# Performance work log

Hardware: AMD Instinct MI355X
Metric: run time of the kernel (lower is better)

Reference implementation:

```python
import jax, jax.numpy as jnp
import numpy as np

C_STD = 64                 # len(standard_1020)
CH_NUMS = (1, 4, 16, 64)   # multi-scale channel counts (ms_ch_lst / ch_nums)
BETA = 0.25
DECAY = 0.99
RESI = 0.5                 # abs(quant_resi) for shared Phi


def l2norm(t, eps=1e-12):
    return t / jnp.maximum(jnp.linalg.norm(t, axis=-1, keepdims=True), eps)


def phi_apply(h_LND, w, b):
    # Phi: y = (1-r)*h + r*Conv1d(h), conv over the channel-position axis, feature dim D
    x = jnp.swapaxes(h_LND, 1, 2)                      # (L, D, Nch)
    y = jax.lax.conv_general_dilated(x, w, (1,), 'SAME',
                                     dimension_numbers=('NCH', 'OIH', 'NCH'))
    y = y + b[None, :, None]
    y = jnp.swapaxes(y, 1, 2)                          # (L, Nch, D)
    return h_LND * (1.0 - RESI) + y * RESI


def setup_inputs() -> dict:
    key = jax.random.key(0)
    ks = jax.random.split(key, 5)
    B, T, D, V = 64, 16, 256, 8192
    N = T * C_STD
    z = jax.random.normal(ks[0], (B, N, D), jnp.float32)
    # per-sample permutation of the 64 standard channel ids in the first C_STD slots
    perm = jnp.argsort(jax.random.uniform(ks[1], (B, C_STD)), axis=1).astype(jnp.int32)
    input_chans = jnp.concatenate([perm, jnp.zeros((B, N - C_STD), jnp.int32)], axis=1)
    # tokens ordered time-major: token j has time index j // C_STD
    input_time = jnp.broadcast_to((jnp.arange(N) // C_STD)[None, :], (B, N)).astype(jnp.int32)
    embedding = jax.random.normal(ks[2], (V, D), jnp.float32) * (D ** -0.5 / 36.0)
    phi_w = jax.random.normal(ks[3], (D, D, 3), jnp.float32) * (1.0 / np.sqrt(3.0 * D))
    phi_b = jnp.zeros((D,), jnp.float32)
    cluster_size = jnp.zeros((V,), jnp.float32)
    return {"z": z, "input_chans": input_chans, "input_time": input_time,
            "embedding": embedding, "phi_w": phi_w, "phi_b": phi_b,
            "cluster_size": cluster_size}


def reference(z, input_chans, input_time, embedding, phi_w, phi_b, cluster_size):
    B, N, D = z.shape
    T = N // C_STD
    V = embedding.shape[0]
    z = l2norm(z)
    chans = input_chans[:, :C_STD]                     # (B, 64) channel ids
    # ch_trans: scatter tokens into standard channel layout -> (L, C_STD, D), L = B*T
    z_btcd = z.reshape(B, T, C_STD, D)
    z_LND = jax.vmap(lambda zb, cb: jnp.zeros((T, C_STD, D), z.dtype).at[:, cb].set(zb))(z_btcd, chans)
    z_LND = z_LND.reshape(B * T, C_STD, D)
    L = B * T

    f_no_grad = jax.lax.stop_gradient(z_LND)
    f_rest = f_no_grad
    f_hat = jnp.zeros_like(f_rest)
    e_n = l2norm(embedding)                            # normalized codebook (V, D)

    SN = len(CH_NUMS)
    loss = jnp.zeros((), z.dtype)
    counts = jnp.zeros((V,), z.dtype)
    idx_list = []
    for g in CH_NUMS:                                  # multi-scale residual VQ over channels
        rest_g = f_rest.reshape(L, g, C_STD // g, D).mean(axis=2)   # group_chans_by_mean
        q = l2norm(rest_g)
        logits = jnp.einsum('lgd,vd->lgv', q, e_n)     # cosine sim == -0.5*l2 dist + const
        idx = jnp.argmax(logits, axis=-1)              # (L, g)
        idx_list.append(idx)
        h_g = e_n[idx]                                 # codebook lookup (L, g, D)
        h = jnp.repeat(h_g, C_STD // g, axis=1)        # expand_chans_by_copy -> (L, 64, D)
        h = phi_apply(h, phi_w, phi_b)                 # shared Phi residual conv
        f_hat = f_hat + h
        f_rest = f_rest - h
        loss = loss + BETA * jnp.mean((jax.lax.stop_gradient(f_hat) - z_LND) ** 2) \
                    + jnp.mean((f_hat - f_no_grad) ** 2)
        counts = counts.at[idx.reshape(-1)].add(1.0)   # EMA cluster-size scatter
    loss = loss / SN

    # straight-through: value = f_hat, gradient flows to z
    f_hat_st = jax.lax.stop_gradient(f_hat) + (z_LND - f_no_grad)
    # ch_intrans: gather back to original per-sample channel ordering
    zq_btcd = jax.vmap(lambda fb, cb: fb[:, cb])(f_hat_st.reshape(B, T, C_STD, D), chans)
    z_q = zq_btcd.reshape(B, N, D)

    cluster_size_new = DECAY * cluster_size + (1.0 - DECAY) * counts
    idx_all = jnp.concatenate(idx_list, axis=1)        # (L, sum(CH_NUMS))
    return z_q, loss, idx_all, cluster_size_new
```

## Files before the change

kernel.cpp:

```cpp
#include <hip/hip_runtime.h>

#define D_DIM 256
#define V_DIM 8192
#define L_DIM 1024
#define NROW 65536
#define NELEM 16777216

#define OUT_LOSS 16777216
#define OUT_IDX  16777217
#define OUT_CS   16864257

#define EN_OFF    ((size_t)0)
#define ENH_OFF   ((size_t)2097152)
#define ESUM_OFF  ((size_t)3145728)
#define E0_OFF    ((size_t)5242880)
#define E2_OFF    ((size_t)7340032)
#define WSUM_OFF  ((size_t)9437184)
#define W0_OFF    ((size_t)9502720)
#define W2_OFF    ((size_t)9568256)
#define FREST_OFF ((size_t)9633792)
#define QF_OFF    ((size_t)26411008)
#define QH_OFF    ((size_t)43188224)
#define PTOP_OFF  ((size_t)51576832)
#define IDXI_OFF  ((size_t)52625408)
#define CNT_OFF   ((size_t)52712448)
#define LOSSP_OFF ((size_t)52720640)
#define RNORM_OFF ((size_t)52722688)
#define INV_OFF   ((size_t)52788224)

typedef __attribute__((ext_vector_type(8))) short bf16x8;
typedef __attribute__((ext_vector_type(4))) float f32x4;

__device__ __forceinline__ unsigned int umaxu(unsigned int a, unsigned int b) { return a > b ? a : b; }
__device__ __forceinline__ unsigned int uminu(unsigned int a, unsigned int b) { return a < b ? a : b; }

__device__ __forceinline__ unsigned short f2b(float x) {
    unsigned int u = __float_as_uint(x);
    unsigned int r = (u + 0x7FFFu + ((u >> 16) & 1u)) >> 16;
    return (unsigned short)r;
}

__device__ __forceinline__ void gl_lds16(const void* g, void* l) {
    __builtin_amdgcn_global_load_lds(
        (const __attribute__((address_space(1))) unsigned int*)g,
        (__attribute__((address_space(3))) unsigned int*)l, 16, 0, 0);
}

__device__ __forceinline__ float blk_reduce_sum(float v, float* sb) {
#pragma unroll
    for (int off = 32; off; off >>= 1) v += __shfl_down(v, off, 64);
    const int w = threadIdx.x >> 6;
    if ((threadIdx.x & 63) == 0) sb[w] = v;
    __syncthreads();
    return sb[0] + sb[1] + sb[2] + sb[3];
}

__global__ void k_norm_embed(const float* __restrict__ emb, float* __restrict__ en,
                             unsigned short* __restrict__ enh) {
    __shared__ float sb[4];
    const int v = blockIdx.x, o = threadIdx.x;
    const float x = emb[(size_t)v * 256 + o];
    const float ss = blk_reduce_sum(x * x, sb);
    const float sc = 1.0f / fmaxf(sqrtf(ss), 1e-12f);
    const float y = x * sc;
    en[(size_t)v * 256 + o] = y;
    enh[(size_t)v * 256 + o] = f2b(y);
}

__global__ void k_prep_w(const float* __restrict__ pw, float* __restrict__ wsum,
                         float* __restrict__ w0, float* __restrict__ w2) {
    const int i = blockIdx.x * 256 + threadIdx.x;
    const float a = pw[(size_t)i * 3 + 0];
    const float b = pw[(size_t)i * 3 + 1];
    const float c = pw[(size_t)i * 3 + 2];
    wsum[i] = a + b + c; w0[i] = a; w2[i] = c;
}

__global__ __launch_bounds__(256) void k_phi_gemm(
    const float* __restrict__ en, const float* __restrict__ wsum,
    const float* __restrict__ w0, const float* __restrict__ w2,
    float* __restrict__ esum, float* __restrict__ e0, float* __restrict__ e2) {
    __shared__ __align__(16) float smem[4096];
    float (*As)[128] = (float (*)[128])smem;
    float (*Bs)[128] = (float (*)[128])(smem + 2048);
    const float* Bm; float* Cm;
    if (blockIdx.z == 0)      { Bm = wsum; Cm = esum; }
    else if (blockIdx.z == 1) { Bm = w0;   Cm = e0;   }
    else                      { Bm = w2;   Cm = e2;   }
    const int tid = threadIdx.x, tx = tid & 15, ty = tid >> 4;
    const int rowbase = blockIdx.x * 128, colbase = blockIdx.y * 128;
    float acc[8][8];
#pragma unroll
    for (int r = 0; r < 8; r++)
#pragma unroll
        for (int c = 0; c < 8; c++) acc[r][c] = 0.f;
    for (int kb = 0; kb < 256; kb += 16) {
        __syncthreads();
        {
            const int lr = tid >> 1, k0 = (tid & 1) << 3;
            const float4* ap = (const float4*)(en + ((size_t)(rowbase + lr)) * 256 + kb + k0);
            const float4 a0 = ap[0], a1 = ap[1];
            const float4* bp = (const float4*)(Bm + ((size_t)(colbase + lr)) * 256 + kb + k0);
            const float4 b0 = bp[0], b1 = bp[1];
            As[k0+0][lr]=a0.x; As[k0+1][lr]=a0.y; As[k0+2][lr]=a0.z; As[k0+3][lr]=a0.w;
            As[k0+4][lr]=a1.x; As[k0+5][lr]=a1.y; As[k0+6][lr]=a1.z; As[k0+7][lr]=a1.w;
            Bs[k0+0][lr]=b0.x; Bs[k0+1][lr]=b0.y; Bs[k0+2][lr]=b0.z; Bs[k0+3][lr]=b0.w;
            Bs[k0+4][lr]=b1.x; Bs[k0+5][lr]=b1.y; Bs[k0+6][lr]=b1.z; Bs[k0+7][lr]=b1.w;
        }
        __syncthreads();
#pragma unroll
        for (int k = 0; k < 16; k++) {
            const float4 av0 = *(const float4*)&As[k][ty << 3];
            const float4 av1 = *(const float4*)&As[k][(ty << 3) + 4];
            const float4 bv0 = *(const float4*)&Bs[k][tx << 3];
            const float4 bv1 = *(const float4*)&Bs[k][(tx << 3) + 4];
            const float a[8] = {av0.x, av0.y, av0.z, av0.w, av1.x, av1.y, av1.z, av1.w};
            const float b[8] = {bv0.x, bv0.y, bv0.z, bv0.w, bv1.x, bv1.y, bv1.z, bv1.w};
#pragma unroll
            for (int r = 0; r < 8; r++)
#pragma unroll
                for (int c = 0; c < 8; c++) acc[r][c] = fmaf(a[r], b[c], acc[r][c]);
        }
    }
#pragma unroll
    for (int r = 0; r < 8; r++) {
        float4 o0 = {acc[r][0], acc[r][1], acc[r][2], acc[r][3]};
        float4 o1 = {acc[r][4], acc[r][5], acc[r][6], acc[r][7]};
        float* cp = Cm + ((size_t)(rowbase + (ty << 3) + r)) * 256 + colbase + (tx << 3);
        *(float4*)cp = o0; *(float4*)(cp + 4) = o1;
    }
}

__global__ void k_invperm(const int* __restrict__ ichans, int* __restrict__ inv) {
    const int b = blockIdx.x, c = threadIdx.x;
    inv[(b << 6) + ichans[(b << 10) + c]] = c;
}

__global__ void k_scatter(const float* __restrict__ z, const int* __restrict__ ichans,
                          float* __restrict__ frest, float* __restrict__ rnorm) {
    __shared__ float sb[4];
    const int zrow = blockIdx.x;
    const int b = zrow >> 10, n = zrow & 1023;
    const int t = n >> 6, c = n & 63;
    const int o = threadIdx.x;
    const float x = z[(size_t)zrow * 256 + o];
    const float ss = blk_reduce_sum(x * x, sb);
    const float sc = 1.0f / fmaxf(sqrtf(ss), 1e-12f);
    const int ch = ichans[(b << 10) + c];
    frest[((size_t)(((b << 4) + t) * 64 + ch)) * 256 + o] = x * sc;
    if (o == 0) rnorm[zrow] = sc;
}

__global__ void k_groupq(const float* __restrict__ frest, float* __restrict__ qf,
                         unsigned short* __restrict__ qh, int g, int s) {
    __shared__ float sb[4];
    const int r = blockIdx.x;
    const int l = r / g, j = r - l * g;
    const int o = threadIdx.x;
    const float* base = frest + ((size_t)l * 64 + (size_t)j * s) * 256 + o;
    float acc = 0.f;
    for (int cc = 0; cc < s; cc++) acc += base[(size_t)cc * 256];
    acc *= (1.0f / (float)s);
    const float ss = blk_reduce_sum(acc * acc, sb);
    const float sc = 1.0f / fmaxf(sqrtf(ss), 1e-12f);
    const float qv = acc * sc;
    qf[(size_t)r * 256 + o] = qv;
    qh[(size_t)r * 256 + o] = f2b(qv);
}

__global__ __launch_bounds__(256, 3) void k_amax1(
    const unsigned short* __restrict__ qh, const unsigned short* __restrict__ enh,
    uint2* __restrict__ ptop, int NC, int colsPerChunk) {
    __shared__ unsigned short As[2][4096];
    __shared__ unsigned short Bs[2][4096];
    const int tid = threadIdx.x;
    const int lane = tid & 63;
    const int m = lane & 15, q4 = lane >> 4;
    const int w = tid >> 6;
    const int wr = w >> 1, wc = w & 1;
    const int rowbase = blockIdx.x * 128;
    const int chunk = blockIdx.y;
    const int colbase0 = chunk * colsPerChunk;
    const int srow = tid >> 2, sgr = tid & 3;

    const unsigned short* qa0 = qh + (size_t)(rowbase + srow) * 256 + sgr * 8;
    const unsigned short* qa1 = qa0 + 64 * 256;
    const unsigned short* eb0 = enh + (size_t)srow * 256 + sgr * 8;
    const unsigned short* eb1 = eb0 + 64 * 256;
    const int loff = tid * 8;

    unsigned int t1[4][4], t2[4][4];
    f32x4 acc[4][4];
#pragma unroll
    for (int i = 0; i < 4; i++)
#pragma unroll
        for (int r = 0; r < 4; r++) {
            t1[i][r] = 0u; t2[i][r] = 0u;
            acc[i][r] = (f32x4){1.25f, 1.25f, 1.25f, 1.25f};
        }

    const int nsteps = (colsPerChunk >> 7) * 8;
    {
        gl_lds16(qa0, &As[0][loff]);
        gl_lds16(qa1, &As[0][2048 + loff]);
        const size_t bgo = (size_t)colbase0 * 256;
        gl_lds16(eb0 + bgo, &Bs[0][loff]);
        gl_lds16(eb1 + bgo, &Bs[0][2048 + loff]);
    }
    for (int step = 0; step < nsteps; step++) {
        const int buf = step & 1;
        __syncthreads();
        if (step + 1 < nsteps) {
            const int kb1 = (step + 1) & 7;
            const int tile1 = (step + 1) >> 3;
            gl_lds16(qa0 + kb1 * 32, &As[buf ^ 1][loff]);
            gl_lds16(qa1 + kb1 * 32, &As[buf ^ 1][2048 + loff]);
            const size_t bgo = (size_t)(colbase0 + tile1 * 128) * 256 + kb1 * 32;
            gl_lds16(eb0 + bgo, &Bs[buf ^ 1][loff]);
            gl_lds16(eb1 + bgo, &Bs[buf ^ 1][2048 + loff]);
        }
        bf16x8 af[4], bfr[4];
#pragma unroll
        for (int i = 0; i < 4; i++)
            af[i] = *(const bf16x8*)&As[buf][(wr * 64 + i * 16 + m) * 32 + q4 * 8];
#pragma unroll
        for (int j = 0; j < 4; j++)
            bfr[j] = *(const bf16x8*)&Bs[buf][(wc * 64 + j * 16 + m) * 32 + q4 * 8];
#pragma unroll
        for (int i = 0; i < 4; i++)
#pragma unroll
            for (int j = 0; j < 4; j++)
                acc[i][j] = __builtin_amdgcn_mfma_f32_16x16x32_bf16(af[i], bfr[j], acc[i][j], 0, 0, 0);
        if ((step & 7) == 7) {
            const int colchunk = colbase0 + (step >> 3) * 128;
#pragma unroll
            for (int j = 0; j < 4; j++) {
                const unsigned int ct = 8191u - (unsigned int)(colchunk + wc * 64 + j * 16 + m);
#pragma unroll
                for (int i = 0; i < 4; i++)
#pragma unroll
                    for (int r = 0; r < 4; r++) {
                        const unsigned int cand =
                            (__float_as_uint(acc[i][j][r]) & 0xFFFFE000u) | (ct & 0x1FFFu);
                        const unsigned int nb1 = umaxu(t1[i][r], cand);
                        t2[i][r] = umaxu(t2[i][r], uminu(t1[i][r], cand));
                        t1[i][r] = nb1;
                        acc[i][j][r] = 1.25f;
                    }
            }
        }
    }
    unsigned int mb1[4][4], mb2[4][4];
#pragma unroll
    for (int i = 0; i < 4; i++)
#pragma unroll
        for (int r = 0; r < 4; r++) {
            unsigned int b1 = t1[i][r], b2 = t2[i][r];
#pragma unroll
            for (int d = 1; d < 16; d <<= 1) {
                const unsigned int o1 = (unsigned int)__shfl_xor((int)b1, d, 64);
                const unsigned int o2 = (unsigned int)__shfl_xor((int)b2, d, 64);
                const unsigned int mn = uminu(b1, o1);
                b1 = umaxu(b1, o1);
                b2 = umaxu(mn, umaxu(b2, o2));
            }
            mb1[i][r] = b1; mb2[i][r] = b2;
        }
    __syncthreads();
    uint2* msh = (uint2*)&As[0][0];
    if (wc == 1 && m == 0) {
#pragma unroll
        for (int i = 0; i < 4; i++)
#pragma unroll
            for (int r = 0; r < 4; r++)
                msh[wr * 64 + i * 16 + q4 * 4 + r] = make_uint2(mb1[i][r], mb2[i][r]);
    }
    __syncthreads();
    if (wc == 0 && m == 0) {
#pragma unroll
        for (int i = 0; i < 4; i++)
#pragma unroll
            for (int r = 0; r < 4; r++) {
                const int rl = wr * 64 + i * 16 + q4 * 4 + r;
                const uint2 o = msh[rl];
                unsigned int b1 = mb1[i][r], b2 = mb2[i][r];
                const unsigned int mn = uminu(b1, o.x);
                b1 = umaxu(b1, o.x);
                b2 = umaxu(mn, umaxu(b2, o.y));
                ptop[(size_t)(rowbase + rl) * NC + chunk] = make_uint2(b1, b2);
            }
    }
}

__global__ __launch_bounds__(256) void k_amax2(
    const uint2* __restrict__ ptop, const float* __restrict__ qf,
    const float* __restrict__ en, int* __restrict__ idxout,
    float* __restrict__ counts, int R, int NC) {
    __shared__ uint2 stop;
    __shared__ double swv[4];
    __shared__ int swi[4];
    const int r = blockIdx.x;
    const int tid = threadIdx.x, lane = tid & 63, w = tid >> 6;
    const uint2* pp = ptop + (size_t)r * NC;
    if (w == 0) {
        const uint2 p = (lane < NC) ? pp[lane] : make_uint2(0u, 0u);
        unsigned int b1 = p.x, b2 = p.y;
#pragma unroll
        for (int d = 1; d < 64; d <<= 1) {
            const unsigned int o1 = (unsigned int)__shfl_xor((int)b1, d, 64);
            const unsigned int o2 = (unsigned int)__shfl_xor((int)b2, d, 64);
            const unsigned int mn = uminu(b1, o1);
            b1 = umaxu(b1, o1);
            b2 = umaxu(mn, umaxu(b2, o2));
        }
        if (lane == 0) stop = make_uint2(b1, b2);
    }
    __syncthreads();
    const unsigned int b1 = stop.x, b2 = stop.y;
    const float* qp = qf + (size_t)r * 256;
    const float4 aq = *(const float4*)(qp + lane * 4);
    const bool ambig = (b1 & 0xFFFFE000u) - (b2 & 0xFFFFE000u) < 32768u;
    if (ambig) {
        double bv = -1e300; int bi = 0x7fffffff;
        const int ncand = 2 * NC;
        for (int ci = w; ci < ncand; ci += 4) {
            const uint2 p = pp[ci >> 1];
            const int col = 8191 - (int)(((ci & 1) ? p.y : p.x) & 0x1FFFu);
            const float4 be = *(const float4*)(en + (size_t)col * 256 + lane * 4);
            double s = (double)aq.x * be.x + (double)aq.y * be.y +
                       (double)aq.z * be.z + (double)aq.w * be.w;
#pragma unroll
            for (int d = 1; d < 64; d <<= 1) s += __shfl_xor(s, d, 64);
            if (s > bv || (s == bv && col < bi)) { bv = s; bi = col; }
        }
        if (lane == 0) { swv[w] = bv; swi[w] = bi; }
        __syncthreads();
        if (tid == 0) {
            double bvv = swv[0]; int bii = swi[0];
            for (int i = 1; i < 4; i++)
                if (swv[i] > bvv || (swv[i] == bvv && swi[i] < bii)) { bvv = swv[i]; bii = swi[i]; }
            idxout[r] = bii;
            atomicAdd(&counts[bii], 1.0f);
        }
    } else if (w == 0) {
        const int c1 = 8191 - (int)(b1 & 0x1FFFu);
        const int c2 = 8191 - (int)(b2 & 0x1FFFu);
        const float4 e1 = *(const float4*)(en + (size_t)c1 * 256 + lane * 4);
        const float4 e2v = *(const float4*)(en + (size_t)c2 * 256 + lane * 4);
        double s1 = (double)aq.x * e1.x + (double)aq.y * e1.y +
                    (double)aq.z * e1.z + (double)aq.w * e1.w;
        double s2 = (double)aq.x * e2v.x + (double)aq.y * e2v.y +
                    (double)aq.z * e2v.z + (double)aq.w * e2v.w;
#pragma unroll
        for (int d = 1; d < 64; d <<= 1) { s1 += __shfl_xor(s1, d, 64); s2 += __shfl_xor(s2, d, 64); }
        if (lane == 0) {
            const int best = (s2 > s1 || (s2 == s1 && c2 < c1)) ? c2 : c1;
            idxout[r] = best;
            atomicAdd(&counts[best], 1.0f);
        }
    }
}

__global__ __launch_bounds__(256) void k_epi(
    float* __restrict__ frest, const float* __restrict__ en,
    const float* __restrict__ esum, const float* __restrict__ e0, const float* __restrict__ e2,
    const float* __restrict__ bias, const int* __restrict__ idx,
    int g, int slog, int smask, double* __restrict__ lossp, int rpb,
    int emitQ, float* __restrict__ qf, unsigned short* __restrict__ qh,
    int emitOut, const float* __restrict__ z, const float* __restrict__ rnorm,
    const int* __restrict__ inv, float* __restrict__ out) {
    __shared__ float sb[8];
    const int bid = blockIdx.x;
    const int o = threadIdx.x;
    const int row0 = bid * rpb;
    const int l = row0 >> 6;
    float qacc = 0.f, lsum = 0.f;
    for (int rr = 0; rr < rpb; rr++) {
        const int row = row0 + rr;
        const int ch = row & 63;
        const int j = ch >> slog;
        const int r = l * g + j;
        const int i0 = idx[r];
        const size_t b0 = (size_t)i0 * 256 + o;
        float v = 0.5f * en[b0] + 0.5f * (esum[b0] + bias[o]);
        const int chs = ch & smask;
        if (chs == 0) {
            float t = -e0[b0];
            if (j > 0) t += e0[(size_t)idx[r - 1] * 256 + o];
            v += 0.5f * t;
        }
        if (chs == smask) {
            float t = -e2[b0];
            if (j < g - 1) t += e2[(size_t)idx[r + 1] * 256 + o];
            v += 0.5f * t;
        }
        const float nv = frest[(size_t)row * 256 + o] - v;
        qacc += nv; lsum = fmaf(nv, nv, lsum);
        if (emitOut) {
            const int b = l >> 4, t_ = l & 15;
            const int c = inv[(b << 6) + ch];
            const size_t zr = (size_t)((b << 10) + (t_ << 6) + c);
            out[zr * 256 + o] = z[zr * 256 + o] * rnorm[zr] - nv;
        } else {
            frest[(size_t)row * 256 + o] = nv;
        }
    }
    const float qm = qacc * (1.0f / (float)rpb);
    float a = lsum, bq = qm * qm;
#pragma unroll
    for (int off = 32; off; off >>= 1) {
        a += __shfl_down(a, off, 64);
        bq += __shfl_down(bq, off, 64);
    }
    const int w = o >> 6;
    if ((o & 63) == 0) { sb[w] = a; sb[4 + w] = bq; }
    __syncthreads();
    if (o == 0)
        atomicAdd(&lossp[bid & 255], (double)(sb[0] + sb[1] + sb[2] + sb[3]));
    if (emitQ) {
        const float qs = sb[4] + sb[5] + sb[6] + sb[7];
        const float sc = 1.0f / fmaxf(sqrtf(qs), 1e-12f);
        const float qv = qm * sc;
        qf[(size_t)bid * 256 + o] = qv;
        qh[(size_t)bid * 256 + o] = f2b(qv);
    }
}

__global__ void k_losssum(const double* __restrict__ lossp, float* __restrict__ out) {
    __shared__ double sb[4];
    double s = 0.0;
    for (int i = threadIdx.x; i < 1024; i += 256) s += lossp[i];
#pragma unroll
    for (int off = 32; off; off >>= 1) s += __shfl_down(s, off, 64);
    if ((threadIdx.x & 63) == 0) sb[threadIdx.x >> 6] = s;
    __syncthreads();
    if (threadIdx.x == 0)
        out[OUT_LOSS] = (float)((sb[0] + sb[1] + sb[2] + sb[3]) * (1.25 / 4.0) / 16777216.0);
}

__global__ void k_final(const int* __restrict__ idxi, const float* __restrict__ counts,
                        const float* __restrict__ csin, float* __restrict__ out) {
    const int i = blockIdx.x * 256 + threadIdx.x;
    if (i < 87040) {
        const int l = i / 85, t = i - l * 85;
        int v;
        if (t == 0)       v = idxi[l];
        else if (t < 5)   v = idxi[1024 + l * 4 + (t - 1)];
        else if (t < 21)  v = idxi[5120 + l * 16 + (t - 5)];
        else              v = idxi[21504 + l * 64 + (t - 21)];
        out[OUT_IDX + i] = (float)v;
    } else if (i < 87040 + 8192) {
        const int v = i - 87040;
        out[OUT_CS + v] = 0.99f * csin[v] + 0.01f * counts[v];
    }
}

extern "C" void kernel_launch(void* const* d_in, const int* in_sizes, int n_in,
                              void* d_out, int out_size, void* d_ws, size_t ws_size,
                              hipStream_t stream) {
    (void)in_sizes; (void)n_in; (void)out_size; (void)ws_size;
    const float* z      = (const float*)d_in[0];
    const int*   ichans = (const int*)d_in[1];
    const float* emb    = (const float*)d_in[3];
    const float* phiw   = (const float*)d_in[4];
    const float* phib   = (const float*)d_in[5];
    const float* csin   = (const float*)d_in[6];
    float* ws  = (float*)d_ws;
    float* out = (float*)d_out;

    float* en    = ws + EN_OFF;
    unsigned short* enh = (unsigned short*)(ws + ENH_OFF);
    float* esum  = ws + ESUM_OFF;
    float* e0    = ws + E0_OFF;
    float* e2    = ws + E2_OFF;
    float* wsum  = ws + WSUM_OFF;
    float* w0    = ws + W0_OFF;
    float* w2    = ws + W2_OFF;
    float* frest = ws + FREST_OFF;
    float* qf    = ws + QF_OFF;
    unsigned short* qh = (unsigned short*)(ws + QH_OFF);
    uint2* ptop  = (uint2*)(ws + PTOP_OFF);
    int*   idxi  = (int*)(ws + IDXI_OFF);
    float* counts = ws + CNT_OFF;
    double* lossp = (double*)(ws + LOSSP_OFF);
    float* rnorm = ws + RNORM_OFF;
    int*   inv   = (int*)(ws + INV_OFF);

    hipMemsetAsync(counts, 0, 8192 * sizeof(float) + 1024 * sizeof(double), stream);

    k_norm_embed<<<V_DIM, 256, 0, stream>>>(emb, en, enh);
    k_prep_w<<<256, 256, 0, stream>>>(phiw, wsum, w0, w2);
    k_phi_gemm<<<dim3(V_DIM / 128, 2, 3), 256, 0, stream>>>(en, wsum, w0, w2, esum, e0, e2);
    k_invperm<<<64, 64, 0, stream>>>(ichans, inv);
    k_scatter<<<NROW, 256, 0, stream>>>(z, ichans, frest, rnorm);
    k_groupq<<<L_DIM, 256, 0, stream>>>(frest, qf, qh, 1, 64);

    const int gs[4]    = {1, 4, 16, 64};
    const int ncs[4]   = {64, 32, 16, 8};
    const int cpcs[4]  = {128, 256, 512, 1024};
    const int offs[4]  = {0, 1024, 5120, 21504};
    const int slogs[4] = {6, 4, 2, 0};
    const int rpbs[4]  = {16, 4, 1, 1};
    for (int st = 0; st < 4; st++) {
        const int g = gs[st], s = 64 / g, NC = ncs[st], R = L_DIM * g;
        k_amax1<<<dim3(R / 128, NC), 256, 0, stream>>>(qh, enh, ptop, NC, cpcs[st]);
        k_amax2<<<R, 256, 0, stream>>>(ptop, qf, en, idxi + offs[st], counts, R, NC);
        k_epi<<<NROW / rpbs[st], 256, 0, stream>>>(frest, en, esum, e0, e2, phib,
                                                   idxi + offs[st], g, slogs[st], s - 1,
                                                   lossp + st * 256, rpbs[st],
                                                   (st < 3) ? 1 : 0, qf, qh,
                                                   (st == 3) ? 1 : 0, z, rnorm, inv, out);
    }

    k_losssum<<<1, 256, 0, stream>>>(lossp, out);
    k_final<<<372, 256, 0, stream>>>(idxi, counts, csin, out);
}
```

Baseline: 1.184 ms.

## Keep full A tile resident in LDS and register-prefetch codebook tiles three steps ahead

The k_amax1 argmax GEMM now loads the whole 128x256 query tile into LDS once, instead of re-streaming A slices every k-step. Codebook (B) slices are prefetched into registers three steps ahead and written into a double-buffered LDS slot at the end of each step. This drops repeated A traffic and hides global latency more deeply. The cost is more LDS and registers, so launch bounds drop from 3 to 2 blocks per CU, which lowers occupancy.

```diff
diff --git a/kernel.cpp b/kernel.cpp
--- a/kernel.cpp
+++ b/kernel.cpp
@@ -168,10 +168,10 @@
     qh[(size_t)r * 256 + o] = f2b(qv);
 }
 
-__global__ __launch_bounds__(256, 3) void k_amax1(
+__global__ __launch_bounds__(256, 2) void k_amax1(
     const unsigned short* __restrict__ qh, const unsigned short* __restrict__ enh,
     uint2* __restrict__ ptop, int NC, int colsPerChunk) {
-    __shared__ unsigned short As[2][4096];
+    __shared__ unsigned short As[8][4096];
     __shared__ unsigned short Bs[2][4096];
     const int tid = threadIdx.x;
     const int lane = tid & 63;
@@ -181,13 +181,32 @@
     const int rowbase = blockIdx.x * 128;
     const int chunk = blockIdx.y;
     const int colbase0 = chunk * colsPerChunk;
-    const int srow = tid >> 2, sgr = tid & 3;
-
-    const unsigned short* qa0 = qh + (size_t)(rowbase + srow) * 256 + sgr * 8;
-    const unsigned short* qa1 = qa0 + 64 * 256;
-    const unsigned short* eb0 = enh + (size_t)srow * 256 + sgr * 8;
-    const unsigned short* eb1 = eb0 + 64 * 256;
-    const int loff = tid * 8;
+    const int ntiles = colsPerChunk >> 7;
+    const int nsteps = ntiles << 3;
+
+    {
+        const unsigned short* qa = qh + (size_t)(rowbase + (tid >> 2)) * 256 + (tid & 3) * 8;
+#pragma unroll
+        for (int kb = 0; kb < 8; kb++) {
+            gl_lds16(qa + kb * 32, &As[kb][tid * 8]);
+            gl_lds16(qa + 64 * 256 + kb * 32, &As[kb][2048 + tid * 8]);
+        }
+    }
+
+    uint4 rb[3][2];
+    const int i0 = tid * 2, i1 = i0 + 1;
+    const size_t bg0 = (size_t)(i0 >> 2) * 256 + (i0 & 3) * 8;
+    const size_t bg1 = (size_t)(i1 >> 2) * 256 + (i1 & 3) * 8;
+#define LOADB(s, slot)                                                          \
+    {                                                                           \
+        const unsigned short* bp = enh +                                        \
+            (size_t)(colbase0 + ((s) >> 3) * 128) * 256 + ((s) & 7) * 32;       \
+        rb[slot][0] = *(const uint4*)(bp + bg0);                                \
+        rb[slot][1] = *(const uint4*)(bp + bg1);                                \
+    }
+    LOADB(0, 0) LOADB(1, 1) LOADB(2, 2)
+    *(uint4*)&Bs[0][tid * 16] = rb[0][0];
+    *(uint4*)&Bs[0][tid * 16 + 8] = rb[0][1];
 
     unsigned int t1[4][4], t2[4][4];
     f32x4 acc[4][4];
@@ -199,30 +218,16 @@
             acc[i][r] = (f32x4){1.25f, 1.25f, 1.25f, 1.25f};
         }
 
-    const int nsteps = (colsPerChunk >> 7) * 8;
-    {
-        gl_lds16(qa0, &As[0][loff]);
-        gl_lds16(qa1, &As[0][2048 + loff]);
-        const size_t bgo = (size_t)colbase0 * 256;
-        gl_lds16(eb0 + bgo, &Bs[0][loff]);
-        gl_lds16(eb1 + bgo, &Bs[0][2048 + loff]);
-    }
+    __syncthreads();
+
     for (int step = 0; step < nsteps; step++) {
         const int buf = step & 1;
-        __syncthreads();
-        if (step + 1 < nsteps) {
-            const int kb1 = (step + 1) & 7;
-            const int tile1 = (step + 1) >> 3;
-            gl_lds16(qa0 + kb1 * 32, &As[buf ^ 1][loff]);
-            gl_lds16(qa1 + kb1 * 32, &As[buf ^ 1][2048 + loff]);
-            const size_t bgo = (size_t)(colbase0 + tile1 * 128) * 256 + kb1 * 32;
-            gl_lds16(eb0 + bgo, &Bs[buf ^ 1][loff]);
-            gl_lds16(eb1 + bgo, &Bs[buf ^ 1][2048 + loff]);
-        }
+        const int kb = step & 7;
+        if (step + 3 < nsteps) LOADB(step + 3, step % 3)
         bf16x8 af[4], bfr[4];
 #pragma unroll
         for (int i = 0; i < 4; i++)
-            af[i] = *(const bf16x8*)&As[buf][(wr * 64 + i * 16 + m) * 32 + q4 * 8];
+            af[i] = *(const bf16x8*)&As[kb][(wr * 64 + i * 16 + m) * 32 + q4 * 8];
 #pragma unroll
         for (int j = 0; j < 4; j++)
             bfr[j] = *(const bf16x8*)&Bs[buf][(wc * 64 + j * 16 + m) * 32 + q4 * 8];
@@ -231,7 +236,7 @@
 #pragma unroll
             for (int j = 0; j < 4; j++)
                 acc[i][j] = __builtin_amdgcn_mfma_f32_16x16x32_bf16(af[i], bfr[j], acc[i][j], 0, 0, 0);
-        if ((step & 7) == 7) {
+        if (kb == 7) {
             const int colchunk = colbase0 + (step >> 3) * 128;
 #pragma unroll
             for (int j = 0; j < 4; j++) {
@@ -249,7 +254,14 @@
                     }
             }
         }
-    }
+        if (step + 1 < nsteps) {
+            const int slot = (step + 1) % 3;
+            *(uint4*)&Bs[buf ^ 1][tid * 16] = rb[slot][0];
+            *(uint4*)&Bs[buf ^ 1][tid * 16 + 8] = rb[slot][1];
+        }
+        __syncthreads();
+    }
+#undef LOADB
     unsigned int mb1[4][4], mb2[4][4];
 #pragma unroll
     for (int i = 0; i < 4; i++)
@@ -266,7 +278,6 @@
             }
             mb1[i][r] = b1; mb2[i][r] = b2;
         }
-    __syncthreads();
     uint2* msh = (uint2*)&As[0][0];
     if (wc == 1 && m == 0) {
 #pragma unroll
```

Measured after the change: 1.562 ms. 1.32x slower.
